# Kernel tuning notes

Hardware: AMD Instinct MI355X
Metric: run time of the kernel (lower is better)

## Reference

```python
import jax, jax.numpy as jnp
import numpy as np
from jax import lax

B, F, N = 1024, 512, 8  # batch, feature_dim, num_of_subAttention


def setup_inputs() -> dict:
    key = jax.random.key(0)
    ks = jax.random.split(key, 8)
    sc = 0.02
    return {
        "vx": jax.random.normal(ks[0], (B, F), dtype=jnp.float32),
        "ax": jax.random.normal(ks[1], (B, F), dtype=jnp.float32),
        # stacked per-unit MLP params (N units)
        "W1": jax.random.normal(ks[2], (N, F, 2 * F), dtype=jnp.float32) * sc,
        "b1": jnp.zeros((N, F), jnp.float32),
        "W2": jax.random.normal(ks[3], (N, F, F), dtype=jnp.float32) * sc,
        "b2": jnp.zeros((N, F), jnp.float32),
        # conv pipeline params (OIHW)
        "conv1_w": jax.random.normal(ks[4], (F, F, 3, 3), dtype=jnp.float32) * sc,
        "conv1_b": jnp.zeros((F,), jnp.float32),
        "conv2_w": jax.random.normal(ks[5], (F, F, 3, 3), dtype=jnp.float32) * sc,
        "conv2_b": jnp.zeros((F,), jnp.float32),
    }


def reference(vx, ax, W1, b1, W2, b2, conv1_w, conv1_b, conv2_w, conv2_b):
    # --- N AttentionUnits, vectorized over the unit axis n ---
    x = jnp.concatenate([vx, ax], axis=-1)                      # [B, 2F]
    # Dropout(0.5) is identity in eval mode.
    h = jax.nn.relu(jnp.einsum('bi,nfi->bnf', x, W1) + b1)      # [B, N, F]
    att = jax.nn.relu(jnp.einsum('bnf,ngf->bng', h, W2) + b2)   # [B, N, F]

    # vx broadcast over units, elementwise attention, then permute to [B, F, N]
    va = jnp.transpose(vx[:, None, :] * att, (0, 2, 1))         # [B, F, N]
    # rank-1 broadcast along trailing axis -> conv input [B, F, N, N]
    t = jnp.broadcast_to(va[..., None], (B, F, N, N))

    dn = ('NCHW', 'OIHW', 'NCHW')
    y = lax.conv_general_dilated(t, conv1_w, (1, 1), 'SAME', dimension_numbers=dn)
    y = y + conv1_b[None, :, None, None]
    k = N // 2
    y = lax.reduce_window(y, -jnp.inf, lax.max, (1, 1, k, k), (1, 1, k, k), 'VALID')  # [B,F,2,2]
    y = lax.conv_general_dilated(y, conv2_w, (1, 1), 'SAME', dimension_numbers=dn)
    y = y + conv2_b[None, :, None, None]
    y = jnp.mean(y, axis=(2, 3))                                # AdaptiveAvgPool2d((1,1)) -> [B, F]
    return jax.nn.relu(y)
```

## Files before the change

### kernel.cpp

```cpp
#include <hip/hip_runtime.h>
#include <hip/hip_bf16.h>


typedef __attribute__((ext_vector_type(8))) short short8;
typedef __attribute__((ext_vector_type(4))) float f32x4;

__device__ __forceinline__ void gload16(const void* g, void* l) {
    __builtin_amdgcn_global_load_lds(
        (const __attribute__((address_space(1))) void*)g,
        (__attribute__((address_space(3))) void*)l, 16, 0, 0);
}

template<int BM, int BN, bool RELU, bool BIAS, bool OUT_BF16, bool SWAP>
__global__ __launch_bounds__(256) void gemm_mfma(
    const __hip_bfloat16* __restrict__ A, int lda, long sA,
    const __hip_bfloat16* __restrict__ B, int ldb, long sB,
    void* __restrict__ Cv, int ldc, long sC,
    const float* __restrict__ bias, long sBias,
    int K)
{
    constexpr int MI = BM / 32, NI = BN / 32;
    constexpr int GA = BM / 16, GB = BN / 16;
    constexpr int nA = (GA * 2) / 4, nB = (GB * 2) / 4;
    __shared__ __align__(16) char As[128 * BM];
    __shared__ __align__(16) char Bs[128 * BN];

    const int z = blockIdx.z;
    A += (long)z * sA;
    B += (long)z * sB;
    const int bm = (SWAP ? blockIdx.x : blockIdx.y) * BM;
    const int bn = (SWAP ? blockIdx.y : blockIdx.x) * BN;
    const int t = threadIdx.x, lane = t & 63, wid = t >> 6;
    const int q = lane >> 4, lr = lane & 15;
    const int wrow = (wid >> 1) * (BM / 2), wcol = (wid & 1) * (BN / 2);

    const int m_loc = lane >> 2;
    const int cst = ((lane & 3) - (m_loc >> 1)) & 3;
    const long abase = ((long)(bm + m_loc) * lda + cst * 8) * 2;
    const long bbase = ((long)(bn + m_loc) * ldb + cst * 8) * 2;
    const int ro = lr * 4;
    const int csel = (lr >> 1);

    f32x4 acc[MI][NI] = {};

    for (int k0 = 0; k0 < K; k0 += 64) {
        if (k0) __syncthreads();
        #pragma unroll
        for (int i = 0; i < nA; ++i) {
            int s = wid * nA + i, g = s % GA, h = s / GA;
            gload16((const char*)A + abase + ((long)g * 16 * lda + h * 32 + k0) * 2,
                    As + (h * (BM * 4) + g * 64) * 16);
        }
        #pragma unroll
        for (int i = 0; i < nB; ++i) {
            int s = wid * nB + i, g = s % GB, h = s / GB;
            gload16((const char*)B + bbase + ((long)g * 16 * ldb + h * 32 + k0) * 2,
                    Bs + (h * (BN * 4) + g * 64) * 16);
        }
        __syncthreads();

        #pragma unroll
        for (int ks = 0; ks < 2; ++ks) {
            short8 af[MI], bf[NI];
            #pragma unroll
            for (int mi = 0; mi < MI; ++mi) {
                int u = ks * (BM * 4) + ((wrow >> 4) + mi) * 64 + ro + ((q + csel) & 3);
                af[mi] = *(const short8*)(As + u * 16);
            }
            #pragma unroll
            for (int ni = 0; ni < NI; ++ni) {
                int u = ks * (BN * 4) + ((wcol >> 4) + ni) * 64 + ro + ((q + csel) & 3);
                bf[ni] = *(const short8*)(Bs + u * 16);
            }
            #pragma unroll
            for (int mi = 0; mi < MI; ++mi)
                #pragma unroll
                for (int ni = 0; ni < NI; ++ni)
                    acc[mi][ni] = __builtin_amdgcn_mfma_f32_16x16x32_bf16(
                        af[mi], bf[ni], acc[mi][ni], 0, 0, 0);
        }
    }

    #pragma unroll
    for (int mi = 0; mi < MI; ++mi) {
        #pragma unroll
        for (int ni = 0; ni < NI; ++ni) {
            int gn = bn + wcol + ni * 16 + lr;
            float bv = 0.f;
            if constexpr (BIAS) bv = bias[z * sBias + gn];
            #pragma unroll
            for (int r = 0; r < 4; ++r) {
                long gm = bm + wrow + mi * 16 + q * 4 + r;
                float v = acc[mi][ni][r] + bv;
                if constexpr (RELU) v = fmaxf(v, 0.f);
                if constexpr (OUT_BF16)
                    ((__hip_bfloat16*)Cv)[z * sC + gm * ldc + gn] = __float2bfloat16(v);
                else
                    ((float*)Cv)[z * sC + gm * ldc + gn] = v;
            }
        }
    }
}

__global__ __launch_bounds__(256) void conv_gemm_pool(
    const __hip_bfloat16* __restrict__ A,
    const __hip_bfloat16* __restrict__ B,
    float* __restrict__ PM)
{
    constexpr int BM = 128, BN = 128, MI = 4, NI = 4;
    constexpr int GA = 8, GB = 8, nA = 4, nB = 4;
    const int lda = 1536, ldb = 1536, K = 1536;
    __shared__ __align__(16) char As[128 * BM];
    __shared__ __align__(16) char Bs[128 * BN];

    const int bm = blockIdx.x * BM;
    const int bn = blockIdx.y * BN;
    const int t = threadIdx.x, lane = t & 63, wid = t >> 6;
    const int q = lane >> 4, lr = lane & 15;
    const int wrow = (wid >> 1) * 64, wcol = (wid & 1) * 64;

    const int m_loc = lane >> 2;
    const int cst = ((lane & 3) - (m_loc >> 1)) & 3;
    const long abase = ((long)(bm + m_loc) * lda + cst * 8) * 2;
    const long bbase = ((long)(bn + m_loc) * ldb + cst * 8) * 2;
    const int ro = lr * 4;
    const int csel = (lr >> 1);

    f32x4 acc[MI][NI] = {};

    for (int k0 = 0; k0 < K; k0 += 64) {
        if (k0) __syncthreads();
        #pragma unroll
        for (int i = 0; i < nA; ++i) {
            int s = wid * nA + i, g = s % GA, h = s / GA;
            gload16((const char*)A + abase + ((long)g * 16 * lda + h * 32 + k0) * 2,
                    As + (h * (BM * 4) + g * 64) * 16);
        }
        #pragma unroll
        for (int i = 0; i < nB; ++i) {
            int s = wid * nB + i, g = s % GB, h = s / GB;
            gload16((const char*)B + bbase + ((long)g * 16 * ldb + h * 32 + k0) * 2,
                    Bs + (h * (BN * 4) + g * 64) * 16);
        }
        __syncthreads();

        #pragma unroll
        for (int ks = 0; ks < 2; ++ks) {
            short8 af[MI], bf[NI];
            #pragma unroll
            for (int mi = 0; mi < MI; ++mi) {
                int u = ks * (BM * 4) + ((wrow >> 4) + mi) * 64 + ro + ((q + csel) & 3);
                af[mi] = *(const short8*)(As + u * 16);
            }
            #pragma unroll
            for (int ni = 0; ni < NI; ++ni) {
                int u = ks * (BN * 4) + ((wcol >> 4) + ni) * 64 + ro + ((q + csel) & 3);
                bf[ni] = *(const short8*)(Bs + u * 16);
            }
            #pragma unroll
            for (int mi = 0; mi < MI; ++mi)
                #pragma unroll
                for (int ni = 0; ni < NI; ++ni)
                    acc[mi][ni] = __builtin_amdgcn_mfma_f32_16x16x32_bf16(
                        af[mi], bf[ni], acc[mi][ni], 0, 0, 0);
        }
    }

    #pragma unroll
    for (int mi = 0; mi < MI; ++mi) {
        int rowbase = bm + wrow + mi * 16;
        int batch = (rowbase >> 3) + (q >> 1);
        int pi = q & 1;
        #pragma unroll
        for (int ni = 0; ni < NI; ++ni) {
            int gn = bn + wcol + ni * 16 + lr;
            int v = gn >> 9, o = gn & 511;
            float m = fmaxf(fmaxf(acc[mi][ni][0], acc[mi][ni][1]),
                            fmaxf(acc[mi][ni][2], acc[mi][ni][3]));
            PM[((long)v * 1024 + batch) * 1024 + pi * 512 + o] = m;
        }
    }
}

__global__ void im2col_kernel(const float* __restrict__ vx,
                              const __hip_bfloat16* __restrict__ att,
                              __hip_bfloat16* __restrict__ A1)
{
    int col = blockIdx.x * 256 + threadIdx.x;
    int row = blockIdx.y;
    int b = row >> 3, i = row & 7;
    int ki = col >> 9, c = col & 511;
    int ip = i + ki - 1;
    float v = 0.f;
    if (ip >= 0 && ip < 8)
        v = vx[(b << 9) + c] * __bfloat162float(att[((long)b << 12) + (ip << 9) + c]);
    A1[(long)row * 1536 + col] = __float2bfloat16(v);
}

__global__ __launch_bounds__(256) void prep_kernel(
    const float* __restrict__ vx, const float* __restrict__ ax,
    const float* __restrict__ W1, const float* __restrict__ W2,
    const float* __restrict__ c1w, const float* __restrict__ c2w,
    __hip_bfloat16* __restrict__ X,  __hip_bfloat16* __restrict__ W1b,
    __hip_bfloat16* __restrict__ W2b, __hip_bfloat16* __restrict__ WC,
    __hip_bfloat16* __restrict__ M2)
{
    int blk = blockIdx.x, t = threadIdx.x;
    if (blk < 2048) {
        int i = blk * 256 + t, b = i >> 9, c = i & 511;
        X[((long)b << 10) + c]       = __float2bfloat16(vx[i]);
        X[((long)b << 10) + 512 + c] = __float2bfloat16(ax[i]);
    } else if (blk < 8192) {
        int j = (blk - 2048) * 256 + t;
        const float* src = (j < 1048576) ? W1 : W2;
        __hip_bfloat16* dst = (j < 1048576) ? W1b : W2b;
        int k = (j < 1048576) ? j : j - 1048576;
        float4 v = ((const float4*)src)[k];
        union { __hip_bfloat16 h[4]; short4 s; } u;
        u.h[0] = __float2bfloat16(v.x); u.h[1] = __float2bfloat16(v.y);
        u.h[2] = __float2bfloat16(v.z); u.h[3] = __float2bfloat16(v.w);
        ((short4*)dst)[k] = u.s;
    } else if (blk < 17408) {
        int b2 = blk - 8192;
        int row = b2 / 6, col = (b2 % 6) * 256 + t;
        int v = row >> 9, o = row & 511;
        int ki = col >> 9, c = col & 511;
        const float* w = c1w + ((long)(o * 512 + c) * 3 + ki) * 3;
        float s = w[1];
        if (v != 0) s += w[0];
        if (v != 2) s += w[2];
        WC[(long)row * 1536 + col] = __float2bfloat16(s);
    } else {
        int b2 = blk - 17408;
        int o2 = b2 >> 3, col = (b2 & 7) * 256 + t;
        int c = col >> 2, pi = (col >> 1) & 1, pj = col & 1;
        const float* w = c2w + (long)(o2 * 512 + c) * 9;
        float s = w[pi * 3 + pj] + w[pi * 3 + pj + 1]
                + w[(pi + 1) * 3 + pj] + w[(pi + 1) * 3 + pj + 1];
        M2[(long)o2 * 2048 + col] = __float2bfloat16(0.25f * s);
    }
}

__global__ __launch_bounds__(256) void combine_kernel(
    const float* __restrict__ PM, const float* __restrict__ c1b,
    __hip_bfloat16* __restrict__ P)
{
    int idx = blockIdx.x * 256 + threadIdx.x;
    int b = idx >> 9, o = idx & 511;
    float bias = c1b[o];
    const long vs = 1024L * 1024;
    long base = (long)b * 1024 + o;
    float l0 = PM[base],            l1 = PM[base + 512];
    float m0 = PM[vs + base],       m1 = PM[vs + base + 512];
    float r0 = PM[2 * vs + base],   r1 = PM[2 * vs + base + 512];
    union { __hip_bfloat16 h[4]; short4 s; } u;
    u.h[0] = __float2bfloat16(fmaxf(l0, m0) + bias);
    u.h[1] = __float2bfloat16(fmaxf(m0, r0) + bias);
    u.h[2] = __float2bfloat16(fmaxf(l1, m1) + bias);
    u.h[3] = __float2bfloat16(fmaxf(m1, r1) + bias);
    ((short4*)(P + (long)b * 2048 + o * 4))[0] = u.s;
}

extern "C" void kernel_launch(void* const* d_in, const int* in_sizes, int n_in,
                              void* d_out, int out_size, void* d_ws, size_t ws_size,
                              hipStream_t stream)
{
    const float* vx  = (const float*)d_in[0];
    const float* ax  = (const float*)d_in[1];
    const float* W1  = (const float*)d_in[2];
    const float* b1  = (const float*)d_in[3];
    const float* W2  = (const float*)d_in[4];
    const float* b2  = (const float*)d_in[5];
    const float* c1w = (const float*)d_in[6];
    const float* c1b = (const float*)d_in[7];
    const float* c2w = (const float*)d_in[8];
    const float* c2b = (const float*)d_in[9];
    float* out = (float*)d_out;
    char* w = (char*)d_ws;

    const long MiB = 1 << 20;
    __hip_bfloat16* Xbf   = (__hip_bfloat16*)(w + 0 * MiB);
    __hip_bfloat16* W1bf  = (__hip_bfloat16*)(w + 2 * MiB);
    __hip_bfloat16* Hbf   = (__hip_bfloat16*)(w + 10 * MiB);
    __hip_bfloat16* W2bf  = (__hip_bfloat16*)(w + 18 * MiB);
    __hip_bfloat16* ATTbf = (__hip_bfloat16*)(w + 22 * MiB);
    __hip_bfloat16* A1bf  = (__hip_bfloat16*)(w + 30 * MiB);
    __hip_bfloat16* WCbf  = (__hip_bfloat16*)(w + 54 * MiB);
    float*          PM    = (float*)         (w + 59 * MiB);
    __hip_bfloat16* Pbf   = (__hip_bfloat16*)(w + 71 * MiB);
    __hip_bfloat16* M2bf  = (__hip_bfloat16*)(w + 75 * MiB);

    prep_kernel<<<21504, 256, 0, stream>>>(vx, ax, W1, W2, c1w, c2w,
                                           Xbf, W1bf, W2bf, WCbf, M2bf);

    gemm_mfma<128, 128, true, true, true, false><<<dim3(32, 8, 1), 256, 0, stream>>>(
        Xbf, 1024, 0, W1bf, 1024, 0, Hbf, 4096, 0, b1, 0, 1024);

    gemm_mfma<128, 128, true, true, true, false><<<dim3(4, 8, 8), 256, 0, stream>>>(
        Hbf, 4096, 512, W2bf, 512, 262144, ATTbf, 4096, 512, b2, 512, 512);

    im2col_kernel<<<dim3(6, 8192), 256, 0, stream>>>(vx, ATTbf, A1bf);

    conv_gemm_pool<<<dim3(64, 12), 256, 0, stream>>>(A1bf, WCbf, PM);

    combine_kernel<<<2048, 256, 0, stream>>>(PM, c1b, Pbf);

    gemm_mfma<64, 64, true, true, false, false><<<dim3(8, 16, 1), 256, 0, stream>>>(
        Pbf, 2048, 0, M2bf, 2048, 0, out, 512, 0, c2b, 0, 2048);
}
```

Before: 223.7 us.

## Fuse im2col into conv GEMM by building A tiles on the fly

Removes the separate im2col kernel and its 24 MiB bf16 intermediate buffer. The conv GEMM now computes vx*att products for each A tile directly into LDS, using register loads instead of async global-to-LDS copies. This saves the round trip through global memory, at the cost of synchronous loads and conversion math inside the GEMM main loop. It also drops an unused SWAP template parameter.

```diff
diff --git a/kernel.cpp b/kernel.cpp
--- a/kernel.cpp
+++ b/kernel.cpp
@@ -11,7 +11,7 @@
         (__attribute__((address_space(3))) void*)l, 16, 0, 0);
 }
 
-template<int BM, int BN, bool RELU, bool BIAS, bool OUT_BF16, bool SWAP>
+template<int BM, int BN, bool RELU, bool BIAS, bool OUT_BF16>
 __global__ __launch_bounds__(256) void gemm_mfma(
     const __hip_bfloat16* __restrict__ A, int lda, long sA,
     const __hip_bfloat16* __restrict__ B, int ldb, long sB,
@@ -28,8 +28,8 @@
     const int z = blockIdx.z;
     A += (long)z * sA;
     B += (long)z * sB;
-    const int bm = (SWAP ? blockIdx.x : blockIdx.y) * BM;
-    const int bn = (SWAP ? blockIdx.y : blockIdx.x) * BN;
+    const int bm = blockIdx.y * BM;
+    const int bn = blockIdx.x * BN;
     const int t = threadIdx.x, lane = t & 63, wid = t >> 6;
     const int q = lane >> 4, lr = lane & 15;
     const int wrow = (wid >> 1) * (BM / 2), wcol = (wid & 1) * (BN / 2);
@@ -103,13 +103,14 @@
 }
 
 __global__ __launch_bounds__(256) void conv_gemm_pool(
-    const __hip_bfloat16* __restrict__ A,
+    const float* __restrict__ vx,
+    const __hip_bfloat16* __restrict__ att,
     const __hip_bfloat16* __restrict__ B,
     float* __restrict__ PM)
 {
     constexpr int BM = 128, BN = 128, MI = 4, NI = 4;
-    constexpr int GA = 8, GB = 8, nA = 4, nB = 4;
-    const int lda = 1536, ldb = 1536, K = 1536;
+    constexpr int GB = 8, nB = 4;
+    const int ldb = 1536;
     __shared__ __align__(16) char As[128 * BM];
     __shared__ __align__(16) char Bs[128 * BN];
 
@@ -120,27 +121,57 @@
     const int wrow = (wid >> 1) * 64, wcol = (wid & 1) * 64;
 
     const int m_loc = lane >> 2;
-    const int cst = ((lane & 3) - (m_loc >> 1)) & 3;
-    const long abase = ((long)(bm + m_loc) * lda + cst * 8) * 2;
-    const long bbase = ((long)(bn + m_loc) * ldb + cst * 8) * 2;
+    const int cstB = ((lane & 3) - (m_loc >> 1)) & 3;
+    const long bbase = ((long)(bn + m_loc) * ldb + cstB * 8) * 2;
     const int ro = lr * 4;
     const int csel = (lr >> 1);
 
+    int lh[4], lrow[4], lkc[4];
+    #pragma unroll
+    for (int u = 0; u < 4; ++u) {
+        int l = t + u * 256;
+        lh[u]   = l >> 9;
+        int r16 = (l >> 2) & 15;
+        lrow[u] = ((l >> 6) & 7) * 16 + r16;
+        lkc[u]  = ((l & 3) - (r16 >> 1)) & 3;
+    }
+
     f32x4 acc[MI][NI] = {};
 
-    for (int k0 = 0; k0 < K; k0 += 64) {
-        if (k0) __syncthreads();
-        #pragma unroll
-        for (int i = 0; i < nA; ++i) {
-            int s = wid * nA + i, g = s % GA, h = s / GA;
-            gload16((const char*)A + abase + ((long)g * 16 * lda + h * 32 + k0) * 2,
-                    As + (h * (BM * 4) + g * 64) * 16);
-        }
+    for (int kk = 0; kk < 24; ++kk) {
+        const int ki = kk >> 3;
+        const int c0 = (kk & 7) << 6;
+        const int k0 = kk << 6;
+        if (kk) __syncthreads();
         #pragma unroll
         for (int i = 0; i < nB; ++i) {
             int s = wid * nB + i, g = s % GB, h = s / GB;
             gload16((const char*)B + bbase + ((long)g * 16 * ldb + h * 32 + k0) * 2,
                     Bs + (h * (BN * 4) + g * 64) * 16);
+        }
+        #pragma unroll
+        for (int u = 0; u < 4; ++u) {
+            int l = t + u * 256;
+            int gm = bm + lrow[u];
+            int b = gm >> 3, ii = gm & 7;
+            int ip = ii + ki - 1;
+            int c = c0 + lh[u] * 32 + lkc[u] * 8;
+            short8 val = {0, 0, 0, 0, 0, 0, 0, 0};
+            if (ip >= 0 && ip < 8) {
+                short8 a8 = *(const short8*)(att + (((long)b << 12) + (ip << 9) + c));
+                const float* vp = vx + (b << 9) + c;
+                float4 v0 = *(const float4*)vp;
+                float4 v1 = *(const float4*)(vp + 4);
+                float vf[8] = {v0.x, v0.y, v0.z, v0.w, v1.x, v1.y, v1.z, v1.w};
+                #pragma unroll
+                for (int j = 0; j < 8; ++j) {
+                    union { short s; __hip_bfloat16 h; } ua; ua.s = a8[j];
+                    union { __hip_bfloat16 h; short s; } ub;
+                    ub.h = __float2bfloat16(__bfloat162float(ua.h) * vf[j]);
+                    val[j] = ub.s;
+                }
+            }
+            *(short8*)(As + l * 16) = val;
         }
         __syncthreads();
 
@@ -180,21 +211,6 @@
             PM[((long)v * 1024 + batch) * 1024 + pi * 512 + o] = m;
         }
     }
-}
-
-__global__ void im2col_kernel(const float* __restrict__ vx,
-                              const __hip_bfloat16* __restrict__ att,
-                              __hip_bfloat16* __restrict__ A1)
-{
-    int col = blockIdx.x * 256 + threadIdx.x;
-    int row = blockIdx.y;
-    int b = row >> 3, i = row & 7;
-    int ki = col >> 9, c = col & 511;
-    int ip = i + ki - 1;
-    float v = 0.f;
-    if (ip >= 0 && ip < 8)
-        v = vx[(b << 9) + c] * __bfloat162float(att[((long)b << 12) + (ip << 9) + c]);
-    A1[(long)row * 1536 + col] = __float2bfloat16(v);
 }
 
 __global__ __launch_bounds__(256) void prep_kernel(
@@ -284,27 +300,24 @@
     __hip_bfloat16* Hbf   = (__hip_bfloat16*)(w + 10 * MiB);
     __hip_bfloat16* W2bf  = (__hip_bfloat16*)(w + 18 * MiB);
     __hip_bfloat16* ATTbf = (__hip_bfloat16*)(w + 22 * MiB);
-    __hip_bfloat16* A1bf  = (__hip_bfloat16*)(w + 30 * MiB);
-    __hip_bfloat16* WCbf  = (__hip_bfloat16*)(w + 54 * MiB);
-    float*          PM    = (float*)         (w + 59 * MiB);
-    __hip_bfloat16* Pbf   = (__hip_bfloat16*)(w + 71 * MiB);
-    __hip_bfloat16* M2bf  = (__hip_bfloat16*)(w + 75 * MiB);
+    __hip_bfloat16* WCbf  = (__hip_bfloat16*)(w + 30 * MiB);
+    float*          PM    = (float*)         (w + 35 * MiB);
+    __hip_bfloat16* Pbf   = (__hip_bfloat16*)(w + 47 * MiB);
+    __hip_bfloat16* M2bf  = (__hip_bfloat16*)(w + 51 * MiB);
 
     prep_kernel<<<21504, 256, 0, stream>>>(vx, ax, W1, W2, c1w, c2w,
                                            Xbf, W1bf, W2bf, WCbf, M2bf);
 
-    gemm_mfma<128, 128, true, true, true, false><<<dim3(32, 8, 1), 256, 0, stream>>>(
+    gemm_mfma<128, 128, true, true, true><<<dim3(32, 8, 1), 256, 0, stream>>>(
         Xbf, 1024, 0, W1bf, 1024, 0, Hbf, 4096, 0, b1, 0, 1024);
 
-    gemm_mfma<128, 128, true, true, true, false><<<dim3(4, 8, 8), 256, 0, stream>>>(
+    gemm_mfma<128, 128, true, true, true><<<dim3(4, 8, 8), 256, 0, stream>>>(
         Hbf, 4096, 512, W2bf, 512, 262144, ATTbf, 4096, 512, b2, 512, 512);
 
-    im2col_kernel<<<dim3(6, 8192), 256, 0, stream>>>(vx, ATTbf, A1bf);
-
-    conv_gemm_pool<<<dim3(64, 12), 256, 0, stream>>>(A1bf, WCbf, PM);
+    conv_gemm_pool<<<dim3(64, 12), 256, 0, stream>>>(vx, ATTbf, WCbf, PM);
 
     combine_kernel<<<2048, 256, 0, stream>>>(PM, c1b, Pbf);
 
-    gemm_mfma<64, 64, true, true, false, false><<<dim3(8, 16, 1), 256, 0, stream>>>(
+    gemm_mfma<64, 64, true, true, false><<<dim3(8, 16, 1), 256, 0, stream>>>(
         Pbf, 2048, 0, M2bf, 2048, 0, out, 512, 0, c2b, 0, 2048);
 }
```

Measured after the change: 224.1 us. About the same (+0.2%).
